# Kernel optimization log

Measured on AMD Instinct MI355X. Metric: run time of the kernel, lower is better.

Reference implementation:

```python
import jax, jax.numpy as jnp
import numpy as np

NEG_SLOPE = 0.2

def _linear(x, w, b):
    return x @ w.T + b

def _encode(samples, w1, b1, w2, b2, lnw, lnb):
    t = samples[:, :, 0:1] / 10000.0
    a = samples[:, :, 1:2] / 20000.0
    x = jnp.concatenate([t, a], axis=2)
    x = jax.nn.relu(_linear(x, w1, b1))
    x = jax.nn.relu(_linear(x, w2, b2))
    mu = x.mean(-1, keepdims=True)
    var = x.var(-1, keepdims=True)
    x = (x - mu) / jnp.sqrt(var + 1e-5) * lnw + lnb
    mask = (jnp.abs(samples).sum(2) > 0).astype(x.dtype)
    denom = jnp.clip(mask.sum(1, keepdims=True), 1e-6, None)
    return (x * mask[:, :, None]).sum(1) / denom

def _gatv2(x, src, dst, edge_attr, wl, bl, wr, br, we, att, bias, H, C):
    N = x.shape[0]
    # PyG add_self_loops with fill_value='mean': self-loop edge_attr = mean of incoming edge_attr per node
    ones = jnp.ones((edge_attr.shape[0],), x.dtype)
    cnt = jax.ops.segment_sum(ones, dst, num_segments=N)
    ea_mean = jax.ops.segment_sum(edge_attr, dst, num_segments=N) / jnp.maximum(cnt, 1.0)[:, None]
    loop = jnp.arange(N, dtype=src.dtype)
    src2 = jnp.concatenate([src, loop])
    dst2 = jnp.concatenate([dst, loop])
    ea2 = jnp.concatenate([edge_attr, ea_mean], axis=0)
    xl = _linear(x, wl, bl).reshape(N, H, C)   # source transform
    xr = _linear(x, wr, br).reshape(N, H, C)   # target transform
    ee = (ea2 @ we.T).reshape(-1, H, C)        # edge conditioning (no bias in PyG lin_edge)
    z = xl[src2] + xr[dst2] + ee               # [E2, H, C]
    z = jnp.where(z > 0, z, NEG_SLOPE * z)     # leaky_relu(0.2)
    logit = jnp.einsum('ehc,hc->eh', z, att)   # [E2, H]
    m = jax.ops.segment_max(logit, dst2, num_segments=N)
    a = jnp.exp(logit - m[dst2])
    denom = jax.ops.segment_sum(a, dst2, num_segments=N)
    a = a / (denom[dst2] + 1e-16)              # PyG softmax eps
    out = jax.ops.segment_sum(xl[src2] * a[:, :, None], dst2, num_segments=N)
    return out.mean(axis=1) + bias             # concat=False -> head mean, then bias


def setup_inputs():
    key = jax.random.key(0)
    ks = jax.random.split(key, 32)
    N, S, E = 30000, 50, 400000
    ED, GD, H = 32, 64, 4
    def w(k, shape, s=0.1):
        return jax.random.normal(k, shape, jnp.float32) * s
    return {
        "samples": jax.random.normal(ks[0], (N, S, 2), jnp.float32),
        "edge_index": jax.random.randint(ks[1], (2, E), 0, N, dtype=jnp.int32),
        "edge_attr": jax.random.normal(ks[2], (E, 1), jnp.float32),
        "enc_fc1_w": w(ks[3], (ED, 2)), "enc_fc1_b": w(ks[4], (ED,)),
        "enc_fc2_w": w(ks[5], (ED, ED)), "enc_fc2_b": w(ks[6], (ED,)),
        "enc_ln_w": jnp.ones((ED,), jnp.float32), "enc_ln_b": jnp.zeros((ED,), jnp.float32),
        "g1_wl": w(ks[7], (H * GD, ED)), "g1_bl": w(ks[8], (H * GD,)),
        "g1_wr": w(ks[9], (H * GD, ED)), "g1_br": w(ks[10], (H * GD,)),
        "g1_we": w(ks[11], (H * GD, 1)), "g1_att": w(ks[12], (H, GD)),
        "g1_bias": w(ks[13], (GD,)),
        "g2_wl": w(ks[14], (H * GD, GD)), "g2_bl": w(ks[15], (H * GD,)),
        "g2_wr": w(ks[16], (H * GD, GD)), "g2_br": w(ks[17], (H * GD,)),
        "g2_we": w(ks[18], (H * GD, 1)), "g2_att": w(ks[19], (H, GD)),
        "g2_bias": w(ks[20], (GD,)),
        "head_w": w(ks[21], (2, GD)), "head_b": w(ks[22], (2,)),
    }


def reference(samples, edge_index, edge_attr,
              enc_fc1_w, enc_fc1_b, enc_fc2_w, enc_fc2_b, enc_ln_w, enc_ln_b,
              g1_wl, g1_bl, g1_wr, g1_br, g1_we, g1_att, g1_bias,
              g2_wl, g2_bl, g2_wr, g2_br, g2_we, g2_att, g2_bias,
              head_w, head_b):
    H, GD = 4, 64
    src, dst = edge_index[0], edge_index[1]
    x = _encode(samples, enc_fc1_w, enc_fc1_b, enc_fc2_w, enc_fc2_b, enc_ln_w, enc_ln_b)
    x = jax.nn.relu(_gatv2(x, src, dst, edge_attr, g1_wl, g1_bl, g1_wr, g1_br, g1_we, g1_att, g1_bias, H, GD))
    x = jax.nn.relu(_gatv2(x, src, dst, edge_attr, g2_wl, g2_bl, g2_wr, g2_br, g2_we, g2_att, g2_bias, H, GD))
    out = _linear(x, head_w, head_b)
    Q = out[:, 0]
    logv = jnp.clip(out[:, 1], -5.0, 10.0)
    return (Q, logv)
```

## Files before the change

kernel.cpp:

```cpp
#include <hip/hip_runtime.h>
#include <hip/hip_fp16.h>
#include <math.h>

#define NSAMP 50
#define ED 32
#define GD 64
#define NH 4
#define STRIDE 40

typedef _Float16 f16;
typedef f16 f16x4 __attribute__((ext_vector_type(4)));
typedef f16 f16x8 __attribute__((ext_vector_type(8)));
typedef float f32x4 __attribute__((ext_vector_type(4)));
typedef f16 h2v __attribute__((ext_vector_type(2)));

__device__ __forceinline__ float red16(float x) {
    int t;
    t = __builtin_amdgcn_update_dpp(0, __float_as_int(x), 0x121, 0xF, 0xF, false);
    x += __int_as_float(t);
    t = __builtin_amdgcn_update_dpp(0, __float_as_int(x), 0x122, 0xF, 0xF, false);
    x += __int_as_float(t);
    t = __builtin_amdgcn_update_dpp(0, __float_as_int(x), 0x124, 0xF, 0xF, false);
    x += __int_as_float(t);
    t = __builtin_amdgcn_update_dpp(0, __float_as_int(x), 0x128, 0xF, 0xF, false);
    x += __int_as_float(t);
    return x;
}

__global__ __launch_bounds__(256) void encode_mfma_kernel(
    const float* __restrict__ samples,
    const float* __restrict__ w1, const float* __restrict__ b1,
    const float* __restrict__ w2, const float* __restrict__ b2,
    const float* __restrict__ lnw, const float* __restrict__ lnb,
    __half* __restrict__ x0h, int N)
{
    int lane = threadIdx.x & 63, wv = threadIdx.x >> 6;
    int n = blockIdx.x * 4 + wv;
    if (n >= N) return;
    int cl = lane & 15, kg = lane >> 4;

    f16x8 af[2];
#pragma unroll
    for (int ct = 0; ct < 2; ct++) {
        const float* wrow = w2 + (size_t)(ct * 16 + cl) * ED;
        float4 lo4 = *(const float4*)(wrow + kg * 4);
        float4 hi4 = *(const float4*)(wrow + 16 + kg * 4);
        f16x8 ah;
        ah[0] = (f16)lo4.x; ah[1] = (f16)lo4.y; ah[2] = (f16)lo4.z; ah[3] = (f16)lo4.w;
        ah[4] = (f16)hi4.x; ah[5] = (f16)hi4.y; ah[6] = (f16)hi4.z; ah[7] = (f16)hi4.w;
        af[ct] = ah;
    }
    float4 bias0 = *(const float4*)(b2 + kg * 4);
    float4 bias1 = *(const float4*)(b2 + 16 + kg * 4);
    float4 wp0 = *(const float4*)(w1 + 8 * kg);
    float4 wp1 = *(const float4*)(w1 + 8 * kg + 4);
    float4 wp2 = *(const float4*)(w1 + 32 + 8 * kg);
    float4 wp3 = *(const float4*)(w1 + 32 + 8 * kg + 4);
    float4 b1lo = *(const float4*)(b1 + 4 * kg);
    float4 b1hi = *(const float4*)(b1 + 16 + 4 * kg);
    const float w1a[8] = {wp0.x, wp0.z, wp1.x, wp1.z, wp2.x, wp2.z, wp3.x, wp3.z};
    const float w1b[8] = {wp0.y, wp0.w, wp1.y, wp1.w, wp2.y, wp2.w, wp3.y, wp3.w};
    const float b1v[8] = {b1lo.x, b1lo.y, b1lo.z, b1lo.w, b1hi.x, b1hi.y, b1hi.z, b1hi.w};

    float P1a[4] = {0.f, 0.f, 0.f, 0.f};
    float P1b[4] = {0.f, 0.f, 0.f, 0.f};
    float P2 = 0.f, W = 0.f;

#pragma unroll
    for (int t = 0; t < 4; t++) {
        int slot = t * 16 + cl;
        float rt = 0.f, ra = 0.f;
        if (slot < NSAMP) {
            float2 v = *(const float2*)(samples + ((size_t)n * NSAMP + slot) * 2);
            rt = v.x; ra = v.y;
        }
        float msk = (fabsf(rt) + fabsf(ra)) > 0.f ? 1.f : 0.f;
        float xi0 = rt * 1e-4f, xi1 = ra * 5e-5f;

        f16x8 bf_;
#pragma unroll
        for (int i = 0; i < 8; i++) {
            float h1 = fmaxf(fmaf(w1a[i], xi0, fmaf(w1b[i], xi1, b1v[i])), 0.f);
            bf_[i] = (f16)h1;
        }

        f32x4 c0 = {bias0.x, bias0.y, bias0.z, bias0.w};
        f32x4 c1 = {bias1.x, bias1.y, bias1.z, bias1.w};
        c0 = __builtin_amdgcn_mfma_f32_16x16x32_f16(af[0], bf_, c0, 0, 0, 0);
        c1 = __builtin_amdgcn_mfma_f32_16x16x32_f16(af[1], bf_, c1, 0, 0, 0);

        float s = 0.f, q = 0.f;
#pragma unroll
        for (int r = 0; r < 4; r++) {
            float h0 = fmaxf(c0[r], 0.f), h1v = fmaxf(c1[r], 0.f);
            c0[r] = h0; c1[r] = h1v;
            s += h0 + h1v;
            q = fmaf(h0, h0, fmaf(h1v, h1v, q));
        }
        s += __shfl_xor(s, 16); s += __shfl_xor(s, 32);
        q += __shfl_xor(q, 16); q += __shfl_xor(q, 32);

        float mu  = s * (1.f / 32.f);
        float var = fmaf(-mu, mu, q * (1.f / 32.f));
        float inv = 1.f / sqrtf(var + 1e-5f);
        float a   = inv * msk;
        P2 = fmaf(-mu, a, P2);
        W += msk;
#pragma unroll
        for (int r = 0; r < 4; r++) {
            P1a[r] = fmaf(a, c0[r], P1a[r]);
            P1b[r] = fmaf(a, c1[r], P1b[r]);
        }
    }

#pragma unroll
    for (int off = 1; off <= 8; off <<= 1) {
#pragma unroll
        for (int r = 0; r < 4; r++) {
            P1a[r] += __shfl_xor(P1a[r], off);
            P1b[r] += __shfl_xor(P1b[r], off);
        }
        P2 += __shfl_xor(P2, off);
        W  += __shfl_xor(W, off);
    }
    if (cl == 0) {
        float rr = 1.f / fmaxf(W, 1e-6f);
        float4 lw0 = *(const float4*)(lnw + kg * 4);
        float4 lb0 = *(const float4*)(lnb + kg * 4);
        float4 lw1 = *(const float4*)(lnw + 16 + kg * 4);
        float4 lb1 = *(const float4*)(lnb + 16 + kg * 4);
        float o0 = (lw0.x * (P1a[0] + P2) + lb0.x * W) * rr;
        float o1 = (lw0.y * (P1a[1] + P2) + lb0.y * W) * rr;
        float o2 = (lw0.z * (P1a[2] + P2) + lb0.z * W) * rr;
        float o3 = (lw0.w * (P1a[3] + P2) + lb0.w * W) * rr;
        float o4 = (lw1.x * (P1b[0] + P2) + lb1.x * W) * rr;
        float o5 = (lw1.y * (P1b[1] + P2) + lb1.y * W) * rr;
        float o6 = (lw1.z * (P1b[2] + P2) + lb1.z * W) * rr;
        float o7 = (lw1.w * (P1b[3] + P2) + lb1.w * W) * rr;
        __half2 h0 = __floats2half2_rn(o0, o1), h1 = __floats2half2_rn(o2, o3);
        __half2 h2 = __floats2half2_rn(o4, o5), h3 = __floats2half2_rn(o6, o7);
        *(uint2*)(x0h + (size_t)n * ED + kg * 4) =
            make_uint2(*(unsigned*)&h0, *(unsigned*)&h1);
        *(uint2*)(x0h + (size_t)n * ED + 16 + kg * 4) =
            make_uint2(*(unsigned*)&h2, *(unsigned*)&h3);
    }
}

__global__ void build_csr_kernel(const int* __restrict__ src, const int* __restrict__ dst,
                                 const float* __restrict__ ea,
                                 int* __restrict__ cnt, float2* __restrict__ csr, int E) {
    int e = blockIdx.x * blockDim.x + threadIdx.x;
    if (e >= E) return;
    int d = dst[e];
    int slot = atomicAdd(&cnt[d], 1);
    if (slot < STRIDE)
        csr[(size_t)d * STRIDE + slot] = make_float2(__int_as_float(src[e] << 9), ea[e]);
}

template <int D>
__global__ __launch_bounds__(256) void xlxr_mfma_kernel(
    const __half* __restrict__ xh,
    const float* __restrict__ wl, const float* __restrict__ bl,
    const float* __restrict__ wr, const float* __restrict__ br,
    __half* __restrict__ xl, __half* __restrict__ xr,
    int nTiles, int tilesPerBlock)
{
    int lane = threadIdx.x & 63, wv = threadIdx.x >> 6;
    int cl = lane & 15, kg = lane >> 4;
    bool isR = blockIdx.y != 0;
    const float* wp = isR ? wr : wl;
    const float* bp = isR ? br : bl;
    __half* outp = isR ? xr : xl;
    int colbase = wv * 64;

    const int KS = D / 32;
    f16x8 bf[4][2];
    float bias_[4];
#pragma unroll
    for (int ct = 0; ct < 4; ct++) {
        int col = colbase + ct * 16 + cl;
        bias_[ct] = bp[col];
        const float* wrow = wp + (size_t)col * D;
#pragma unroll
        for (int ks = 0; ks < KS; ks++) {
            float4 lo = *(const float4*)(wrow + ks * 32 + kg * 4);
            float4 hi = *(const float4*)(wrow + ks * 32 + kg * 4 + 16);
            f16x8 bb;
            bb[0] = (f16)lo.x; bb[1] = (f16)lo.y; bb[2] = (f16)lo.z; bb[3] = (f16)lo.w;
            bb[4] = (f16)hi.x; bb[5] = (f16)hi.y; bb[6] = (f16)hi.z; bb[7] = (f16)hi.w;
            bf[ct][ks] = bb;
        }
    }

    int t0 = blockIdx.x * tilesPerBlock;
    int t1 = min(t0 + tilesPerBlock, nTiles);
    for (int t = t0; t < t1; ++t) {
        const __half* rp = xh + ((size_t)(t * 16 + cl)) * D;
        f16x8 a[2];
#pragma unroll
        for (int ks = 0; ks < KS; ks++) {
            f16x4 alo = *(const f16x4*)(rp + ks * 32 + kg * 4);
            f16x4 ahi = *(const f16x4*)(rp + ks * 32 + kg * 4 + 16);
            a[ks] = __builtin_shufflevector(alo, ahi, 0, 1, 2, 3, 4, 5, 6, 7);
        }
        int r0 = t * 16 + kg * 4;
#pragma unroll
        for (int ct = 0; ct < 4; ct++) {
            f32x4 c = {bias_[ct], bias_[ct], bias_[ct], bias_[ct]};
#pragma unroll
            for (int ks = 0; ks < KS; ks++)
                c = __builtin_amdgcn_mfma_f32_16x16x32_f16(a[ks], bf[ct][ks], c, 0, 0, 0);
            int col = colbase + ct * 16 + cl;
#pragma unroll
            for (int i = 0; i < 4; i++)
                outp[(size_t)(r0 + i) * 256 + col] = __float2half(c[i]);
        }
    }
}

template <bool FINAL>
__global__ __launch_bounds__(256) void gat_kernel(
    const __half* __restrict__ xl, const __half* __restrict__ xr,
    const int* __restrict__ cnt_arr, const float2* __restrict__ csr,
    const float* __restrict__ we, const float* __restrict__ att,
    const float* __restrict__ bias,
    const float* __restrict__ hw, const float* __restrict__ hb,
    void* __restrict__ xout, int N)
{
    int lane = threadIdx.x & 63;
    int n = blockIdx.x * 4 + (threadIdx.x >> 6);
    if (n >= N) return;
    const char* xlb = (const char*)xl;
    const uint2* xrh = (const uint2*)xr;
    uint2 xrp = xrh[(size_t)n * 64 + lane];
    h2v xr01 = __builtin_bit_cast(h2v, xrp.x);
    h2v xr23 = __builtin_bit_cast(h2v, xrp.y);
    float4 wev = ((const float4*)we)[lane];
    float4 atv = ((const float4*)att)[lane];
    const float L2E = 1.44269504088896340736f;

    h2v we01, we23, a601, a623, a401, a423;
    we01[0] = (f16)wev.x; we01[1] = (f16)wev.y;
    we23[0] = (f16)wev.z; we23[1] = (f16)wev.w;
    a601[0] = (f16)(atv.x * (0.6f * L2E)); a601[1] = (f16)(atv.y * (0.6f * L2E));
    a623[0] = (f16)(atv.z * (0.6f * L2E)); a623[1] = (f16)(atv.w * (0.6f * L2E));
    a401[0] = (f16)(atv.x * (0.4f * L2E)); a401[1] = (f16)(atv.y * (0.4f * L2E));
    a423[0] = (f16)(atv.z * (0.4f * L2E)); a423[1] = (f16)(atv.w * (0.4f * L2E));

    int cnt_s = __builtin_amdgcn_readfirstlane(cnt_arr[n]);
    int cc = min(cnt_s, STRIDE);

    int vsrc = n << 9; float vea = 0.f;
    if (lane < cc) {
        float2 pr = csr[(size_t)n * STRIDE + lane];
        vsrc = __float_as_int(pr.x);
        vea  = pr.y;
    }

    float sea = 0.f;
    float S0 = 0.f, S1 = 0.f;
    float4 A0 = make_float4(0, 0, 0, 0), A1 = make_float4(0, 0, 0, 0);

    uint2 xA[4], xB[4];
    float eA[4], eB[4];
    int laneoff = lane * 8;

    auto fetchg = [&](int k0, uint2* xv, float* ev) {
#pragma unroll
        for (int c = 0; c < 4; ++c) {
            int k = k0 + c;
            int off = __builtin_amdgcn_readlane(vsrc, k);
            ev[c] = __int_as_float(__builtin_amdgcn_readlane(__float_as_int(vea), k));
            xv[c] = *(const uint2*)(xlb + off + laneoff);
        }
    };
    auto edge = [&](int k, uint2 xc, float e, float& S, float4& A) {
        sea += e;
        h2v x01 = __builtin_bit_cast(h2v, xc.x);
        h2v x23 = __builtin_bit_cast(h2v, xc.y);
        h2v e2 = __builtin_bit_cast(h2v, __builtin_amdgcn_cvt_pkrtz(e, e));
        h2v z01 = e2 * we01 + (x01 + xr01);
        h2v z23 = e2 * we23 + (x23 + xr23);
        h2v az01 = __builtin_bit_cast(h2v, __builtin_bit_cast(int, z01) & 0x7FFF7FFF);
        h2v az23 = __builtin_bit_cast(h2v, __builtin_bit_cast(int, z23) & 0x7FFF7FFF);
        float part = __builtin_amdgcn_fdot2(a601, z01, 0.f, false);
        part = __builtin_amdgcn_fdot2(a623, z23, part, false);
        part = __builtin_amdgcn_fdot2(a401, az01, part, false);
        part = __builtin_amdgcn_fdot2(a423, az23, part, false);
        part = red16(part);
        float p = exp2f(part);
        p = (k < cc) ? p : 0.f;
        S += p;
        A.x = fmaf(p, (float)x01[0], A.x);
        A.y = fmaf(p, (float)x01[1], A.y);
        A.z = fmaf(p, (float)x23[0], A.z);
        A.w = fmaf(p, (float)x23[1], A.w);
    };
    auto procg = [&](int k0, const uint2* xv, const float* ev) {
        edge(k0 + 0, xv[0], ev[0], S0, A0);
        edge(k0 + 1, xv[1], ev[1], S1, A1);
        edge(k0 + 2, xv[2], ev[2], S0, A0);
        edge(k0 + 3, xv[3], ev[3], S1, A1);
    };

    uint2 xself = *(const uint2*)(xlb + ((size_t)n << 9) + laneoff);

    int ngrp = (cc + 3) >> 2;
    if (ngrp > 0) {
        fetchg(0, xA, eA);
        int g = 0;
        while (true) {
            if (g + 1 < ngrp) fetchg((g + 1) * 4, xB, eB);
            procg(g * 4, xA, eA);
            if (++g >= ngrp) break;
            if (g + 1 < ngrp) fetchg((g + 1) * 4, xA, eA);
            procg(g * 4, xB, eB);
            if (++g >= ngrp) break;
        }
    }

    float eself = sea / fmaxf((float)cnt_s, 1.f);
    edge(-1, xself, eself, S0, A0);

    float S = S0 + S1;
    float4 A = make_float4(A0.x + A1.x, A0.y + A1.y, A0.z + A1.z, A0.w + A1.w);

    float inv = 1.f / S;
    float ox = A.x * inv, oy = A.y * inv, oz = A.z * inv, ow = A.w * inv;
    ox += __shfl_xor(ox, 16); ox += __shfl_xor(ox, 32);
    oy += __shfl_xor(oy, 16); oy += __shfl_xor(oy, 32);
    oz += __shfl_xor(oz, 16); oz += __shfl_xor(oz, 32);
    ow += __shfl_xor(ow, 16); ow += __shfl_xor(ow, 32);
    if (lane < 16) {
        float4 bv = ((const float4*)bias)[lane];
        ox = fmaxf(fmaf(ox, 0.25f, bv.x), 0.f);
        oy = fmaxf(fmaf(oy, 0.25f, bv.y), 0.f);
        oz = fmaxf(fmaf(oz, 0.25f, bv.z), 0.f);
        ow = fmaxf(fmaf(ow, 0.25f, bv.w), 0.f);
        if (!FINAL) {
            __half2 h0 = __floats2half2_rn(ox, oy);
            __half2 h1 = __floats2half2_rn(oz, ow);
            uint2 pk = make_uint2(*(unsigned*)&h0, *(unsigned*)&h1);
            *(uint2*)((__half*)xout + (size_t)n * 64 + lane * 4) = pk;
        } else {
            float* outp = (float*)xout;
            int c0 = lane * 4;
            float q = ox * hw[c0] + oy * hw[c0 + 1] + oz * hw[c0 + 2] + ow * hw[c0 + 3];
            float v = ox * hw[64 + c0] + oy * hw[64 + c0 + 1] + oz * hw[64 + c0 + 2] + ow * hw[64 + c0 + 3];
            q += __shfl_xor(q, 1); q += __shfl_xor(q, 2); q += __shfl_xor(q, 4); q += __shfl_xor(q, 8);
            v += __shfl_xor(v, 1); v += __shfl_xor(v, 2); v += __shfl_xor(v, 4); v += __shfl_xor(v, 8);
            if (lane == 0) {
                outp[n]     = q + hb[0];
                outp[N + n] = fminf(fmaxf(v + hb[1], -5.f), 10.f);
            }
        }
    }
}

extern "C" void kernel_launch(void* const* d_in, const int* in_sizes, int n_in,
                              void* d_out, int out_size, void* d_ws, size_t ws_size,
                              hipStream_t stream)
{
    const float* samples    = (const float*)d_in[0];
    const int*   edge_index = (const int*)d_in[1];
    const float* edge_attr  = (const float*)d_in[2];
    const float* e_fc1_w = (const float*)d_in[3];
    const float* e_fc1_b = (const float*)d_in[4];
    const float* e_fc2_w = (const float*)d_in[5];
    const float* e_fc2_b = (const float*)d_in[6];
    const float* e_ln_w  = (const float*)d_in[7];
    const float* e_ln_b  = (const float*)d_in[8];
    const float* g1_wl  = (const float*)d_in[9];
    const float* g1_bl  = (const float*)d_in[10];
    const float* g1_wr  = (const float*)d_in[11];
    const float* g1_br  = (const float*)d_in[12];
    const float* g1_we  = (const float*)d_in[13];
    const float* g1_att = (const float*)d_in[14];
    const float* g1_bias= (const float*)d_in[15];
    const float* g2_wl  = (const float*)d_in[16];
    const float* g2_bl  = (const float*)d_in[17];
    const float* g2_wr  = (const float*)d_in[18];
    const float* g2_br  = (const float*)d_in[19];
    const float* g2_we  = (const float*)d_in[20];
    const float* g2_att = (const float*)d_in[21];
    const float* g2_bias= (const float*)d_in[22];
    const float* head_w = (const float*)d_in[23];
    const float* head_b = (const float*)d_in[24];

    const int N = in_sizes[0] / (NSAMP * 2);
    const int E = in_sizes[2];
    const int* src = edge_index;
    const int* dst = edge_index + E;

    char* p = (char*)d_ws;
    auto take = [&](size_t bytes) { char* r = p; p += (bytes + 255) & ~(size_t)255; return r; };
    int*    cnt  = (int*)take((size_t)N * 4);
    float2* csr  = (float2*)take((size_t)N * STRIDE * 8);
    __half* x0h  = (__half*)take((size_t)N * ED * 2);
    __half* x1h  = (__half*)take((size_t)N * GD * 2);
    __half* xl   = (__half*)take((size_t)N * NH * GD * 2);
    __half* xr   = (__half*)take((size_t)N * NH * GD * 2);
    (void)ws_size; (void)n_in; (void)out_size;

    (void)hipMemsetAsync(cnt, 0, (size_t)N * 4, stream);

    encode_mfma_kernel<<<(N + 3) / 4, 256, 0, stream>>>(samples, e_fc1_w, e_fc1_b,
                                                        e_fc2_w, e_fc2_b,
                                                        e_ln_w, e_ln_b, x0h, N);
    build_csr_kernel<<<(E + 255) / 256, 256, 0, stream>>>(src, dst, edge_attr, cnt, csr, E);

    const int TPB = 5;
    int nTiles = N / 16;
    dim3 mgrid((nTiles + TPB - 1) / TPB, 2);

    xlxr_mfma_kernel<ED><<<mgrid, 256, 0, stream>>>(x0h, g1_wl, g1_bl, g1_wr, g1_br,
                                                    xl, xr, nTiles, TPB);
    gat_kernel<false><<<(N + 3) / 4, 256, 0, stream>>>(xl, xr, cnt, csr, g1_we, g1_att, g1_bias,
                                                       nullptr, nullptr, x1h, N);
    xlxr_mfma_kernel<GD><<<mgrid, 256, 0, stream>>>(x1h, g2_wl, g2_bl, g2_wr, g2_br,
                                                    xl, xr, nTiles, TPB);
    gat_kernel<true><<<(N + 3) / 4, 256, 0, stream>>>(xl, xr, cnt, csr, g2_we, g2_att, g2_bias,
                                                      head_w, head_b, d_out, N);
}
```

Baseline: 181.9 us.

## Pack CSR entries into 32-bit words and launch one wave per node

Each CSR entry becomes a single 32-bit word holding the source index in the high 16 bits and the edge attribute as fp16 in the low bits. This halves CSR traffic and removes a readlane per edge. The self-loop edge-attr mean is now computed up front with a wave reduction, and the tail edges are handled by a scalar remainder loop instead of masking. The GAT kernels launch 64-thread blocks, one per node. The packing limits node indices to 65535 and rounds the edge attribute to fp16.

After: 168.2 us. 1.08x faster.

```diff
diff --git a/kernel.cpp b/kernel.cpp
--- a/kernel.cpp
+++ b/kernel.cpp
@@ -148,13 +148,14 @@
 
 __global__ void build_csr_kernel(const int* __restrict__ src, const int* __restrict__ dst,
                                  const float* __restrict__ ea,
-                                 int* __restrict__ cnt, float2* __restrict__ csr, int E) {
+                                 int* __restrict__ cnt, unsigned* __restrict__ csru, int E) {
     int e = blockIdx.x * blockDim.x + threadIdx.x;
     if (e >= E) return;
     int d = dst[e];
     int slot = atomicAdd(&cnt[d], 1);
     if (slot < STRIDE)
-        csr[(size_t)d * STRIDE + slot] = make_float2(__int_as_float(src[e] << 9), ea[e]);
+        csru[(size_t)d * STRIDE + slot] =
+            ((unsigned)src[e] << 16) | (unsigned)__half_as_ushort(__float2half_rn(ea[e]));
 }
 
 template <int D>
@@ -219,17 +220,16 @@
 }
 
 template <bool FINAL>
-__global__ __launch_bounds__(256) void gat_kernel(
+__global__ __launch_bounds__(64) void gat_kernel(
     const __half* __restrict__ xl, const __half* __restrict__ xr,
-    const int* __restrict__ cnt_arr, const float2* __restrict__ csr,
+    const int* __restrict__ cnt_arr, const unsigned* __restrict__ csru,
     const float* __restrict__ we, const float* __restrict__ att,
     const float* __restrict__ bias,
     const float* __restrict__ hw, const float* __restrict__ hb,
     void* __restrict__ xout, int N)
 {
     int lane = threadIdx.x & 63;
-    int n = blockIdx.x * 4 + (threadIdx.x >> 6);
-    if (n >= N) return;
+    int n = blockIdx.x;
     const char* xlb = (const char*)xl;
     const uint2* xrh = (const uint2*)xr;
     uint2 xrp = xrh[(size_t)n * 64 + lane];
@@ -250,35 +250,36 @@
     int cnt_s = __builtin_amdgcn_readfirstlane(cnt_arr[n]);
     int cc = min(cnt_s, STRIDE);
 
-    int vsrc = n << 9; float vea = 0.f;
-    if (lane < cc) {
-        float2 pr = csr[(size_t)n * STRIDE + lane];
-        vsrc = __float_as_int(pr.x);
-        vea  = pr.y;
-    }
-
-    float sea = 0.f;
+    unsigned upk = (unsigned)n << 16;
+    if (lane < cc) upk = csru[(size_t)n * STRIDE + lane];
+
+    float veaf = __half2float(__ushort_as_half((unsigned short)(upk & 0xFFFFu)));
+    float sea = veaf;
+#pragma unroll
+    for (int off = 1; off <= 32; off <<= 1) sea += __shfl_xor(sea, off);
+    float eself = sea / fmaxf((float)cnt_s, 1.f);
+
     float S0 = 0.f, S1 = 0.f;
     float4 A0 = make_float4(0, 0, 0, 0), A1 = make_float4(0, 0, 0, 0);
 
     uint2 xA[4], xB[4];
-    float eA[4], eB[4];
+    unsigned uA[4], uB[4];
     int laneoff = lane * 8;
 
-    auto fetchg = [&](int k0, uint2* xv, float* ev) {
+    auto fetchg = [&](int k0, uint2* xv, unsigned* uv) {
 #pragma unroll
         for (int c = 0; c < 4; ++c) {
-            int k = k0 + c;
-            int off = __builtin_amdgcn_readlane(vsrc, k);
-            ev[c] = __int_as_float(__builtin_amdgcn_readlane(__float_as_int(vea), k));
+            unsigned u = (unsigned)__builtin_amdgcn_readlane((int)upk, k0 + c);
+            uv[c] = u;
+            int off = (int)((u >> 16) << 9);
             xv[c] = *(const uint2*)(xlb + off + laneoff);
         }
     };
-    auto edge = [&](int k, uint2 xc, float e, float& S, float4& A) {
-        sea += e;
+    auto edgeu = [&](uint2 xc, unsigned u, float& S, float4& A) {
         h2v x01 = __builtin_bit_cast(h2v, xc.x);
         h2v x23 = __builtin_bit_cast(h2v, xc.y);
-        h2v e2 = __builtin_bit_cast(h2v, __builtin_amdgcn_cvt_pkrtz(e, e));
+        unsigned eb = (u & 0xFFFFu) * 0x10001u;
+        h2v e2 = __builtin_bit_cast(h2v, eb);
         h2v z01 = e2 * we01 + (x01 + xr01);
         h2v z23 = e2 * we23 + (x23 + xr23);
         h2v az01 = __builtin_bit_cast(h2v, __builtin_bit_cast(int, z01) & 0x7FFF7FFF);
@@ -289,38 +290,60 @@
         part = __builtin_amdgcn_fdot2(a423, az23, part, false);
         part = red16(part);
         float p = exp2f(part);
-        p = (k < cc) ? p : 0.f;
         S += p;
         A.x = fmaf(p, (float)x01[0], A.x);
         A.y = fmaf(p, (float)x01[1], A.y);
         A.z = fmaf(p, (float)x23[0], A.z);
         A.w = fmaf(p, (float)x23[1], A.w);
     };
-    auto procg = [&](int k0, const uint2* xv, const float* ev) {
-        edge(k0 + 0, xv[0], ev[0], S0, A0);
-        edge(k0 + 1, xv[1], ev[1], S1, A1);
-        edge(k0 + 2, xv[2], ev[2], S0, A0);
-        edge(k0 + 3, xv[3], ev[3], S1, A1);
+    auto procg = [&](const uint2* xv, const unsigned* uv) {
+        edgeu(xv[0], uv[0], S0, A0);
+        edgeu(xv[1], uv[1], S1, A1);
+        edgeu(xv[2], uv[2], S0, A0);
+        edgeu(xv[3], uv[3], S1, A1);
     };
 
     uint2 xself = *(const uint2*)(xlb + ((size_t)n << 9) + laneoff);
 
-    int ngrp = (cc + 3) >> 2;
-    if (ngrp > 0) {
-        fetchg(0, xA, eA);
+    int fullg = cc >> 2, rem = cc & 3;
+    if (fullg > 0) {
+        fetchg(0, xA, uA);
         int g = 0;
         while (true) {
-            if (g + 1 < ngrp) fetchg((g + 1) * 4, xB, eB);
-            procg(g * 4, xA, eA);
-            if (++g >= ngrp) break;
-            if (g + 1 < ngrp) fetchg((g + 1) * 4, xA, eA);
-            procg(g * 4, xB, eB);
-            if (++g >= ngrp) break;
-        }
-    }
-
-    float eself = sea / fmaxf((float)cnt_s, 1.f);
-    edge(-1, xself, eself, S0, A0);
+            if (g + 1 < fullg) fetchg((g + 1) * 4, xB, uB);
+            procg(xA, uA);
+            if (++g >= fullg) break;
+            if (g + 1 < fullg) fetchg((g + 1) * 4, xA, uA);
+            procg(xB, uB);
+            if (++g >= fullg) break;
+        }
+    }
+    for (int k = fullg * 4; k < cc; ++k) {
+        unsigned u = (unsigned)__builtin_amdgcn_readlane((int)upk, k);
+        int off = (int)((u >> 16) << 9);
+        uint2 xc = *(const uint2*)(xlb + off + laneoff);
+        edgeu(xc, u, S0, A0);
+    }
+    {
+        h2v e2 = __builtin_bit_cast(h2v, __builtin_amdgcn_cvt_pkrtz(eself, eself));
+        h2v x01 = __builtin_bit_cast(h2v, xself.x);
+        h2v x23 = __builtin_bit_cast(h2v, xself.y);
+        h2v z01 = e2 * we01 + (x01 + xr01);
+        h2v z23 = e2 * we23 + (x23 + xr23);
+        h2v az01 = __builtin_bit_cast(h2v, __builtin_bit_cast(int, z01) & 0x7FFF7FFF);
+        h2v az23 = __builtin_bit_cast(h2v, __builtin_bit_cast(int, z23) & 0x7FFF7FFF);
+        float part = __builtin_amdgcn_fdot2(a601, z01, 0.f, false);
+        part = __builtin_amdgcn_fdot2(a623, z23, part, false);
+        part = __builtin_amdgcn_fdot2(a401, az01, part, false);
+        part = __builtin_amdgcn_fdot2(a423, az23, part, false);
+        part = red16(part);
+        float p = exp2f(part);
+        S1 += p;
+        A1.x = fmaf(p, (float)x01[0], A1.x);
+        A1.y = fmaf(p, (float)x01[1], A1.y);
+        A1.z = fmaf(p, (float)x23[0], A1.z);
+        A1.w = fmaf(p, (float)x23[1], A1.w);
+    }
 
     float S = S0 + S1;
     float4 A = make_float4(A0.x + A1.x, A0.y + A1.y, A0.z + A1.z, A0.w + A1.w);
@@ -394,12 +417,12 @@
 
     char* p = (char*)d_ws;
     auto take = [&](size_t bytes) { char* r = p; p += (bytes + 255) & ~(size_t)255; return r; };
-    int*    cnt  = (int*)take((size_t)N * 4);
-    float2* csr  = (float2*)take((size_t)N * STRIDE * 8);
-    __half* x0h  = (__half*)take((size_t)N * ED * 2);
-    __half* x1h  = (__half*)take((size_t)N * GD * 2);
-    __half* xl   = (__half*)take((size_t)N * NH * GD * 2);
-    __half* xr   = (__half*)take((size_t)N * NH * GD * 2);
+    int*      cnt  = (int*)take((size_t)N * 4);
+    unsigned* csru = (unsigned*)take((size_t)N * STRIDE * 4);
+    __half*   x0h  = (__half*)take((size_t)N * ED * 2);
+    __half*   x1h  = (__half*)take((size_t)N * GD * 2);
+    __half*   xl   = (__half*)take((size_t)N * NH * GD * 2);
+    __half*   xr   = (__half*)take((size_t)N * NH * GD * 2);
     (void)ws_size; (void)n_in; (void)out_size;
 
     (void)hipMemsetAsync(cnt, 0, (size_t)N * 4, stream);
@@ -407,7 +430,7 @@
     encode_mfma_kernel<<<(N + 3) / 4, 256, 0, stream>>>(samples, e_fc1_w, e_fc1_b,
                                                         e_fc2_w, e_fc2_b,
                                                         e_ln_w, e_ln_b, x0h, N);
-    build_csr_kernel<<<(E + 255) / 256, 256, 0, stream>>>(src, dst, edge_attr, cnt, csr, E);
+    build_csr_kernel<<<(E + 255) / 256, 256, 0, stream>>>(src, dst, edge_attr, cnt, csru, E);
 
     const int TPB = 5;
     int nTiles = N / 16;
@@ -415,10 +438,10 @@
 
     xlxr_mfma_kernel<ED><<<mgrid, 256, 0, stream>>>(x0h, g1_wl, g1_bl, g1_wr, g1_br,
                                                     xl, xr, nTiles, TPB);
-    gat_kernel<false><<<(N + 3) / 4, 256, 0, stream>>>(xl, xr, cnt, csr, g1_we, g1_att, g1_bias,
-                                                       nullptr, nullptr, x1h, N);
+    gat_kernel<false><<<N, 64, 0, stream>>>(xl, xr, cnt, csru, g1_we, g1_att, g1_bias,
+                                            nullptr, nullptr, x1h, N);
     xlxr_mfma_kernel<GD><<<mgrid, 256, 0, stream>>>(x1h, g2_wl, g2_bl, g2_wr, g2_br,
                                                     xl, xr, nTiles, TPB);
-    gat_kernel<true><<<(N + 3) / 4, 256, 0, stream>>>(xl, xr, cnt, csr, g2_we, g2_att, g2_bias,
-                                                      head_w, head_b, d_out, N);
-}
+    gat_kernel<true><<<N, 64, 0, stream>>>(xl, xr, cnt, csru, g2_we, g2_att, g2_bias,
+                                           head_w, head_b, d_out, N);
+}
```
